# Kernel optimization log

Hardware: AMD Instinct MI355X
Metric: run time of the kernel (lower is better)

Reference implementation:

```python
import jax, jax.numpy as jnp
import numpy as np

L, B, S, H = 2, 32, 2048, 512  # layers, batch, src_len, hidden_size
D = 2 * H                      # feature dim of hidden / encoder_outputs


def setup_inputs() -> dict:
    key = jax.random.key(0)
    k1, k2, k3, k4, k5 = jax.random.split(key, 5)
    scale = 1.0 / np.sqrt(4 * H)
    return {
        "hidden": jax.random.normal(k1, (L, B, D), dtype=jnp.float32),
        "encoder_outputs": jax.random.normal(k2, (B, S, D), dtype=jnp.float32),
        "attn_w": jax.random.normal(k3, (H, 4 * H), dtype=jnp.float32) * scale,
        "attn_b": jax.random.normal(k4, (H,), dtype=jnp.float32) * scale,
        "v_w": jax.random.normal(k5, (1, H), dtype=jnp.float32) * (1.0 / np.sqrt(H)),
    }


def reference(hidden, encoder_outputs, attn_w, attn_b, v_w):
    # hidden: [L, B, D]; permute(1,0,2) then [:, -1, :] == last layer state [B, D]
    h = hidden[-1]  # [B, D]
    # Avoid materializing the [B,S,2D] concat: split attn_w into the block acting
    # on the (repeated) hidden part and the block acting on encoder_outputs.
    w_h, w_e = attn_w[:, :D], attn_w[:, D:]          # [H, D] each
    # hidden contribution is constant over src_len -> compute once per batch row
    e_h = jnp.einsum('bd,hd->bh', h, w_h)            # [B, H]
    e_e = jnp.einsum('bsd,hd->bsh', encoder_outputs, w_e)  # [B, S, H]
    energy = jnp.tanh(e_e + e_h[:, None, :] + attn_b)      # [B, S, H]
    scores = jnp.einsum('bsh,h->bs', energy, v_w[0])       # [B, S]
    attention_weights = jax.nn.softmax(scores, axis=1)     # [B, S]
    context = jnp.einsum('bs,bsd->bd', attention_weights, encoder_outputs)
    return (context[:, None, :], attention_weights[:, None, :])
```

## Files before the change

### kernel.cpp

```cpp
#include <hip/hip_runtime.h>
#include <math.h>

#define LL 2
#define BB 32
#define SS 2048
#define HH 512
#define DD 1024
#define W4S 2048

#define BM 64
#define BN 256
#define BK 64
#define NT (DD / BK)

typedef __attribute__((ext_vector_type(8))) short bf16x8;
typedef __attribute__((ext_vector_type(4))) float f32x4;

__device__ inline unsigned pk2_rne(float a, float b) {
    unsigned ua = __float_as_uint(a), ub = __float_as_uint(b);
    unsigned ra = (ua + 0x7fffu + ((ua >> 16) & 1u)) >> 16;
    unsigned rb = (ub + 0x7fffu + ((ub >> 16) & 1u)) & 0xffff0000u;
    return ra | rb;
}

__device__ inline unsigned pk2_hu(float a, float b) {
    unsigned ua = __float_as_uint(a) + 0x8000u;
    unsigned ub = __float_as_uint(b) + 0x8000u;
    return __builtin_amdgcn_perm(ub, ua, 0x07060302u);
}

__device__ inline float fast_tanh(float x) {
    x = fminf(9.f, fmaxf(-9.f, x));
    float e = __expf(2.f * x);
    return 1.f - 2.f * __builtin_amdgcn_rcpf(e + 1.f);
}

__device__ inline void gl_lds16(const unsigned short* g, short* l) {
    __builtin_amdgcn_global_load_lds(
        (const __attribute__((address_space(1))) unsigned int*)g,
        (__attribute__((address_space(3))) unsigned int*)l, 16, 0, 0);
}

__global__ __launch_bounds__(256) void k_prep(const float* __restrict__ hidden,
                                              const float* __restrict__ attn_w,
                                              const float* __restrict__ attn_b,
                                              unsigned short* __restrict__ Bp,
                                              float* __restrict__ base,
                                              float* __restrict__ scores) {
    int bx = blockIdx.x;
    if (bx < BB * SS / 256) {
        scores[bx * 256 + threadIdx.x] = 0.f;
        return;
    }
    bx -= BB * SS / 256;
    if (bx < HH) {
        int t = threadIdx.x;
        float4 v = *(const float4*)(attn_w + (size_t)bx * W4S + DD + t * 4);
        *(uint2*)(Bp + (size_t)bx * DD + t * 4) =
            make_uint2(pk2_rne(v.x, v.y), pk2_rne(v.z, v.w));
        return;
    }
    bx -= HH;
    int wid  = bx * 4 + (threadIdx.x >> 6);
    int lane = threadIdx.x & 63;
    int b = wid >> 9;
    int h = wid & (HH - 1);
    const float4* h4 = (const float4*)(hidden + (size_t)(LL - 1) * BB * DD + (size_t)b * DD);
    const float4* w4 = (const float4*)(attn_w + (size_t)h * W4S);
    float s = 0.f;
    #pragma unroll
    for (int i = 0; i < 4; i++) {
        float4 a = h4[lane + i * 64], w = w4[lane + i * 64];
        s += a.x * w.x + a.y * w.y + a.z * w.z + a.w * w.w;
    }
    #pragma unroll
    for (int off = 32; off; off >>= 1) s += __shfl_xor(s, off);
    if (lane == 0) base[b * HH + h] = s + attn_b[h];
}

__global__ __launch_bounds__(256, 2) void k_scores(const float* __restrict__ enc,
                                                   const unsigned short* __restrict__ Bp,
                                                   const float* __restrict__ base,
                                                   const float* __restrict__ vw,
                                                   float* __restrict__ scores) {
    __shared__ short As[2][8 * 64 * 8];
    __shared__ short Bs[2][4][8 * 64 * 8];

    const int tid  = threadIdx.x;
    const int wid  = tid >> 6;
    const int lane = tid & 63;
    const int lm   = lane & 15;
    const int kq   = lane >> 4;
    const int n0   = blockIdx.x * BN;
    const int m0   = blockIdx.y * BM;
    const int b    = m0 >> 11;
    const int wn   = n0 + wid * 64;

    const float* Ag = enc + (size_t)(m0 + wid * 16 + lm) * DD + kq * 8;
    const unsigned short* Bgl = Bp + (size_t)(wn + lm) * DD + kq * 8;

    #pragma unroll
    for (int ni = 0; ni < 4; ni++)
        #pragma unroll
        for (int s = 0; s < 2; s++)
            gl_lds16(Bgl + (size_t)ni * 16 * DD + s * 32,
                     &Bs[0][wid][(ni * 2 + s) * 64 * 8]);

    float4 ra[2][4];
    #pragma unroll
    for (int s = 0; s < 2; s++) {
        ra[0][s * 2 + 0] = *(const float4*)(Ag + s * 32);
        ra[0][s * 2 + 1] = *(const float4*)(Ag + s * 32 + 4);
        ra[1][s * 2 + 0] = *(const float4*)(Ag + 64 + s * 32);
        ra[1][s * 2 + 1] = *(const float4*)(Ag + 64 + s * 32 + 4);
    }
    #pragma unroll
    for (int s = 0; s < 2; s++) {
        float4 x = ra[0][s * 2], y = ra[0][s * 2 + 1];
        uint4 p = {pk2_hu(x.x, x.y), pk2_hu(x.z, x.w),
                   pk2_hu(y.x, y.y), pk2_hu(y.z, y.w)};
        *(uint4*)&As[0][((wid * 2 + s) * 64 + lane) * 8] = p;
    }

    f32x4 acc[4][4];
    #pragma unroll
    for (int i = 0; i < 4; i++)
        #pragma unroll
        for (int j = 0; j < 4; j++) acc[i][j] = (f32x4){0.f, 0.f, 0.f, 0.f};

    #pragma unroll 2
    for (int kt = 0; kt < NT; kt++) {
        const int c = kt & 1;
        __syncthreads();
        if (kt + 1 < NT) {
            #pragma unroll
            for (int ni = 0; ni < 4; ni++)
                #pragma unroll
                for (int s = 0; s < 2; s++)
                    gl_lds16(Bgl + (size_t)ni * 16 * DD + (kt + 1) * 64 + s * 32,
                             &Bs[c ^ 1][wid][(ni * 2 + s) * 64 * 8]);
            if (kt + 2 < NT) {
                #pragma unroll
                for (int s = 0; s < 2; s++) {
                    ra[c][s * 2 + 0] = *(const float4*)(Ag + (kt + 2) * 64 + s * 32);
                    ra[c][s * 2 + 1] = *(const float4*)(Ag + (kt + 2) * 64 + s * 32 + 4);
                }
            }
            #pragma unroll
            for (int s = 0; s < 2; s++) {
                float4 x = ra[c ^ 1][s * 2], y = ra[c ^ 1][s * 2 + 1];
                uint4 p = {pk2_hu(x.x, x.y), pk2_hu(x.z, x.w),
                           pk2_hu(y.x, y.y), pk2_hu(y.z, y.w)};
                *(uint4*)&As[c ^ 1][((wid * 2 + s) * 64 + lane) * 8] = p;
            }
        }
        #pragma unroll
        for (int s = 0; s < 2; s++) {
            bf16x8 af[4];
            #pragma unroll
            for (int mi = 0; mi < 4; mi++)
                af[mi] = *(const bf16x8*)&As[c][((mi * 2 + s) * 64 + lane) * 8];
            #pragma unroll
            for (int ni = 0; ni < 4; ni++) {
                bf16x8 bf = *(const bf16x8*)&Bs[c][wid][((ni * 2 + s) * 64 + lane) * 8];
                #pragma unroll
                for (int mi = 0; mi < 4; mi++)
                    acc[mi][ni] = __builtin_amdgcn_mfma_f32_16x16x32_bf16(
                        af[mi], bf, acc[mi][ni], 0, 0, 0);
            }
        }
    }

    const float* basep = base + b * HH + wn;
    const float* vp    = vw + wn;
    float p[4][4] = {};
    #pragma unroll
    for (int ni = 0; ni < 4; ni++) {
        int nl = ni * 16 + lm;
        float bs = basep[nl];
        float vv = vp[nl];
        #pragma unroll
        for (int mi = 0; mi < 4; mi++)
            #pragma unroll
            for (int r = 0; r < 4; r++)
                p[mi][r] += vv * fast_tanh(acc[mi][ni][r] + bs);
    }
    #pragma unroll
    for (int off = 8; off; off >>= 1)
        #pragma unroll
        for (int mi = 0; mi < 4; mi++)
            #pragma unroll
            for (int r = 0; r < 4; r++)
                p[mi][r] += __shfl_xor(p[mi][r], off);
    if (lm == 0) {
        #pragma unroll
        for (int mi = 0; mi < 4; mi++)
            #pragma unroll
            for (int r = 0; r < 4; r++)
                atomicAdd(&scores[m0 + mi * 16 + kq * 4 + r], p[mi][r]);
    }
}

__global__ __launch_bounds__(256) void k_smstat(const float* __restrict__ scores,
                                                float2* __restrict__ stat) {
    int b = blockIdx.x, tid = threadIdx.x;
    const float* rowp = scores + b * SS;
    float v[8];
    float m = -1e30f;
    #pragma unroll
    for (int i = 0; i < 8; i++) { v[i] = rowp[tid + i * 256]; m = fmaxf(m, v[i]); }
    __shared__ float sm[4], ssum[4];
    #pragma unroll
    for (int off = 32; off; off >>= 1) m = fmaxf(m, __shfl_xor(m, off));
    if ((tid & 63) == 0) sm[tid >> 6] = m;
    __syncthreads();
    m = fmaxf(fmaxf(sm[0], sm[1]), fmaxf(sm[2], sm[3]));
    float s = 0.f;
    #pragma unroll
    for (int i = 0; i < 8; i++) s += __expf(v[i] - m);
    #pragma unroll
    for (int off = 32; off; off >>= 1) s += __shfl_xor(s, off);
    if ((tid & 63) == 0) ssum[tid >> 6] = s;
    __syncthreads();
    if (tid == 0) {
        float tot = ssum[0] + ssum[1] + ssum[2] + ssum[3];
        stat[b] = make_float2(m, 1.f / tot);
    }
}

#define CCH 64
__global__ __launch_bounds__(256) void k_ctxpart(const float* __restrict__ enc,
                                                 const float* __restrict__ scores,
                                                 const float2* __restrict__ stat,
                                                 float* __restrict__ attn_out,
                                                 float* __restrict__ part) {
    int b = blockIdx.x, c = blockIdx.y, tid = threadIdx.x;
    __shared__ float wsh[CCH];
    float2 st = stat[b];
    if (tid < CCH) {
        float w = __expf(scores[b * SS + c * CCH + tid] - st.x) * st.y;
        wsh[tid] = w;
        attn_out[b * SS + c * CCH + tid] = w;
    }
    __syncthreads();
    const float4* e4 = (const float4*)(enc + ((size_t)b * SS + c * CCH) * DD);
    float4 acc = {0.f, 0.f, 0.f, 0.f};
    #pragma unroll 8
    for (int s = 0; s < CCH; s++) {
        float wv  = wsh[s];
        float4 ev = e4[(size_t)s * (DD / 4) + tid];
        acc.x += wv * ev.x; acc.y += wv * ev.y;
        acc.z += wv * ev.z; acc.w += wv * ev.w;
    }
    *(float4*)(part + (size_t)(b * 32 + c) * DD + tid * 4) = acc;
}

__global__ __launch_bounds__(256) void k_ctxreduce(const float* __restrict__ part,
                                                   float* __restrict__ ctx) {
    int b = blockIdx.x, d = blockIdx.y * 256 + threadIdx.x;
    float s = 0.f;
    #pragma unroll
    for (int c = 0; c < 32; c++) s += part[(size_t)(b * 32 + c) * DD + d];
    ctx[b * DD + d] = s;
}

extern "C" void kernel_launch(void* const* d_in, const int* in_sizes, int n_in,
                              void* d_out, int out_size, void* d_ws, size_t ws_size,
                              hipStream_t stream) {
    const float* hidden = (const float*)d_in[0];
    const float* enc    = (const float*)d_in[1];
    const float* attn_w = (const float*)d_in[2];
    const float* attn_b = (const float*)d_in[3];
    const float* v_w    = (const float*)d_in[4];

    float* out      = (float*)d_out;
    float* ctx_out  = out;
    float* attn_out = out + BB * DD;

    float* base        = (float*)d_ws;
    float* scores      = base + BB * HH;
    unsigned short* Bp = (unsigned short*)(scores + BB * SS);
    float2* stat       = (float2*)(Bp + (size_t)HH * DD);
    float* part        = (float*)(stat + BB);

    hipLaunchKernelGGL(k_prep, dim3(BB * SS / 256 + HH + BB * HH / 4), dim3(256),
                       0, stream, hidden, attn_w, attn_b, Bp, base, scores);
    hipLaunchKernelGGL(k_scores, dim3(2, BB * SS / BM), dim3(256), 0, stream,
                       enc, Bp, base, v_w, scores);
    hipLaunchKernelGGL(k_smstat, dim3(BB), dim3(256), 0, stream, scores, stat);
    hipLaunchKernelGGL(k_ctxpart, dim3(BB, SS / CCH), dim3(256), 0, stream,
                       enc, scores, stat, attn_out, part);
    hipLaunchKernelGGL(k_ctxreduce, dim3(BB, DD / 256), dim3(256), 0, stream,
                       part, ctx_out);
}
```

Before: 521.6 us.

## Retile scores GEMM with BK=32, pre-swizzled weight layout and higher occupancy

Repacks the bf16 weight matrix in the prep kernel into a k-tile-major layout with XOR swizzle, so each wave loads its B tile contiguously with global-to-LDS loads. The A tile load is restructured so each thread converts one float4 per row pair, writing into XOR-swizzled LDS to avoid bank conflicts. K-tile depth is halved to 32 and launch bounds raised to 4 blocks per CU, trading more loop iterations and barriers for smaller LDS use and higher occupancy to hide memory latency.

```diff
diff --git a/kernel.cpp b/kernel.cpp
--- a/kernel.cpp
+++ b/kernel.cpp
@@ -10,7 +10,7 @@
 
 #define BM 64
 #define BN 256
-#define BK 64
+#define BK 32
 #define NT (DD / BK)
 
 typedef __attribute__((ext_vector_type(8))) short bf16x8;
@@ -44,7 +44,7 @@
 __global__ __launch_bounds__(256) void k_prep(const float* __restrict__ hidden,
                                               const float* __restrict__ attn_w,
                                               const float* __restrict__ attn_b,
-                                              unsigned short* __restrict__ Bp,
+                                              unsigned short* __restrict__ BpT,
                                               float* __restrict__ base,
                                               float* __restrict__ scores) {
     int bx = blockIdx.x;
@@ -54,10 +54,12 @@
     }
     bx -= BB * SS / 256;
     if (bx < HH) {
-        int t = threadIdx.x;
-        float4 v = *(const float4*)(attn_w + (size_t)bx * W4S + DD + t * 4);
-        *(uint2*)(Bp + (size_t)bx * DD + t * 4) =
-            make_uint2(pk2_rne(v.x, v.y), pk2_rne(v.z, v.w));
+        int t = threadIdx.x, n = bx;
+        float4 v = *(const float4*)(attn_w + (size_t)n * W4S + DD + t * 4);
+        int kt = t >> 3, g = (t >> 1) & 3, half = t & 1;
+        size_t off = (size_t)kt * (512 * BK) + (size_t)n * BK
+                   + ((g ^ (n & 3)) * 8) + half * 4;
+        *(uint2*)(BpT + off) = make_uint2(pk2_rne(v.x, v.y), pk2_rne(v.z, v.w));
         return;
     }
     bx -= HH;
@@ -78,13 +80,13 @@
     if (lane == 0) base[b * HH + h] = s + attn_b[h];
 }
 
-__global__ __launch_bounds__(256, 2) void k_scores(const float* __restrict__ enc,
-                                                   const unsigned short* __restrict__ Bp,
+__global__ __launch_bounds__(256, 4) void k_scores(const float* __restrict__ enc,
+                                                   const unsigned short* __restrict__ BpT,
                                                    const float* __restrict__ base,
                                                    const float* __restrict__ vw,
                                                    float* __restrict__ scores) {
-    __shared__ short As[2][8 * 64 * 8];
-    __shared__ short Bs[2][4][8 * 64 * 8];
+    __shared__ short As[2][BM * BK];
+    __shared__ short Bs[2][BN * BK];
 
     const int tid  = threadIdx.x;
     const int wid  = tid >> 6;
@@ -96,31 +98,15 @@
     const int b    = m0 >> 11;
     const int wn   = n0 + wid * 64;
 
-    const float* Ag = enc + (size_t)(m0 + wid * 16 + lm) * DD + kq * 8;
-    const unsigned short* Bgl = Bp + (size_t)(wn + lm) * DD + kq * 8;
-
-    #pragma unroll
-    for (int ni = 0; ni < 4; ni++)
-        #pragma unroll
-        for (int s = 0; s < 2; s++)
-            gl_lds16(Bgl + (size_t)ni * 16 * DD + s * 32,
-                     &Bs[0][wid][(ni * 2 + s) * 64 * 8]);
-
-    float4 ra[2][4];
-    #pragma unroll
-    for (int s = 0; s < 2; s++) {
-        ra[0][s * 2 + 0] = *(const float4*)(Ag + s * 32);
-        ra[0][s * 2 + 1] = *(const float4*)(Ag + s * 32 + 4);
-        ra[1][s * 2 + 0] = *(const float4*)(Ag + 64 + s * 32);
-        ra[1][s * 2 + 1] = *(const float4*)(Ag + 64 + s * 32 + 4);
-    }
-    #pragma unroll
-    for (int s = 0; s < 2; s++) {
-        float4 x = ra[0][s * 2], y = ra[0][s * 2 + 1];
-        uint4 p = {pk2_hu(x.x, x.y), pk2_hu(x.z, x.w),
-                   pk2_hu(y.x, y.y), pk2_hu(y.z, y.w)};
-        *(uint4*)&As[0][((wid * 2 + s) * 64 + lane) * 8] = p;
-    }
+    const int rA = tid >> 3;
+    const int gA = tid & 7;
+    const float* Ag0 = enc + (size_t)(m0 + rA) * DD + gA * 4;
+    const float* Ag1 = Ag0 + (size_t)32 * DD;
+    const int wA0 = rA * BK + (((gA >> 1) ^ (rA & 3)) * 8) + (gA & 1) * 4;
+    const int wA1 = (rA + 32) * BK + (((gA >> 1) ^ ((rA + 32) & 3)) * 8) + (gA & 1) * 4;
+
+    const unsigned short* Bgw = BpT + (size_t)(n0 + wid * 64) * BK + lane * 8;
+    short* BsW[2] = { &Bs[0][wid * 64 * BK], &Bs[1][wid * 64 * BK] };
 
     f32x4 acc[4][4];
     #pragma unroll
@@ -128,46 +114,51 @@
         #pragma unroll
         for (int j = 0; j < 4; j++) acc[i][j] = (f32x4){0.f, 0.f, 0.f, 0.f};
 
-    #pragma unroll 2
+    #pragma unroll
+    for (int i = 0; i < 4; i++)
+        gl_lds16(Bgw + (size_t)i * 64 * 8, BsW[0] + i * 64 * 8);
+    float4 ra[2][2];
+    ra[0][0] = *(const float4*)(Ag0);
+    ra[0][1] = *(const float4*)(Ag1);
+    {
+        uint2 p0 = {pk2_hu(ra[0][0].x, ra[0][0].y), pk2_hu(ra[0][0].z, ra[0][0].w)};
+        uint2 p1 = {pk2_hu(ra[0][1].x, ra[0][1].y), pk2_hu(ra[0][1].z, ra[0][1].w)};
+        *(uint2*)&As[0][wA0] = p0;
+        *(uint2*)&As[0][wA1] = p1;
+    }
+    ra[1][0] = *(const float4*)(Ag0 + BK);
+    ra[1][1] = *(const float4*)(Ag1 + BK);
+
     for (int kt = 0; kt < NT; kt++) {
         const int c = kt & 1;
         __syncthreads();
         if (kt + 1 < NT) {
             #pragma unroll
-            for (int ni = 0; ni < 4; ni++)
-                #pragma unroll
-                for (int s = 0; s < 2; s++)
-                    gl_lds16(Bgl + (size_t)ni * 16 * DD + (kt + 1) * 64 + s * 32,
-                             &Bs[c ^ 1][wid][(ni * 2 + s) * 64 * 8]);
+            for (int i = 0; i < 4; i++)
+                gl_lds16(Bgw + (size_t)(kt + 1) * 512 * BK + (size_t)i * 64 * 8,
+                         BsW[c ^ 1] + i * 64 * 8);
+            float4 x = ra[c ^ 1][0], y = ra[c ^ 1][1];
+            uint2 p0 = {pk2_hu(x.x, x.y), pk2_hu(x.z, x.w)};
+            uint2 p1 = {pk2_hu(y.x, y.y), pk2_hu(y.z, y.w)};
+            *(uint2*)&As[c ^ 1][wA0] = p0;
+            *(uint2*)&As[c ^ 1][wA1] = p1;
             if (kt + 2 < NT) {
-                #pragma unroll
-                for (int s = 0; s < 2; s++) {
-                    ra[c][s * 2 + 0] = *(const float4*)(Ag + (kt + 2) * 64 + s * 32);
-                    ra[c][s * 2 + 1] = *(const float4*)(Ag + (kt + 2) * 64 + s * 32 + 4);
-                }
-            }
-            #pragma unroll
-            for (int s = 0; s < 2; s++) {
-                float4 x = ra[c ^ 1][s * 2], y = ra[c ^ 1][s * 2 + 1];
-                uint4 p = {pk2_hu(x.x, x.y), pk2_hu(x.z, x.w),
-                           pk2_hu(y.x, y.y), pk2_hu(y.z, y.w)};
-                *(uint4*)&As[c ^ 1][((wid * 2 + s) * 64 + lane) * 8] = p;
+                ra[c][0] = *(const float4*)(Ag0 + (kt + 2) * BK);
+                ra[c][1] = *(const float4*)(Ag1 + (kt + 2) * BK);
             }
         }
-        #pragma unroll
-        for (int s = 0; s < 2; s++) {
-            bf16x8 af[4];
+        bf16x8 af[4];
+        #pragma unroll
+        for (int mi = 0; mi < 4; mi++)
+            af[mi] = *(const bf16x8*)&As[c][(mi * 16 + lm) * BK + ((kq ^ (lm & 3)) * 8)];
+        #pragma unroll
+        for (int ni = 0; ni < 4; ni++) {
+            bf16x8 bf = *(const bf16x8*)
+                &Bs[c][(wid * 64 + ni * 16 + lm) * BK + ((kq ^ (lm & 3)) * 8)];
             #pragma unroll
             for (int mi = 0; mi < 4; mi++)
-                af[mi] = *(const bf16x8*)&As[c][((mi * 2 + s) * 64 + lane) * 8];
-            #pragma unroll
-            for (int ni = 0; ni < 4; ni++) {
-                bf16x8 bf = *(const bf16x8*)&Bs[c][wid][((ni * 2 + s) * 64 + lane) * 8];
-                #pragma unroll
-                for (int mi = 0; mi < 4; mi++)
-                    acc[mi][ni] = __builtin_amdgcn_mfma_f32_16x16x32_bf16(
-                        af[mi], bf, acc[mi][ni], 0, 0, 0);
-            }
+                acc[mi][ni] = __builtin_amdgcn_mfma_f32_16x16x32_bf16(
+                    af[mi], bf, acc[mi][ni], 0, 0, 0);
         }
     }
 
@@ -277,16 +268,16 @@
     float* ctx_out  = out;
     float* attn_out = out + BB * DD;
 
-    float* base        = (float*)d_ws;
-    float* scores      = base + BB * HH;
-    unsigned short* Bp = (unsigned short*)(scores + BB * SS);
-    float2* stat       = (float2*)(Bp + (size_t)HH * DD);
-    float* part        = (float*)(stat + BB);
+    float* base         = (float*)d_ws;
+    float* scores       = base + BB * HH;
+    unsigned short* BpT = (unsigned short*)(scores + BB * SS);
+    float2* stat        = (float2*)(BpT + (size_t)HH * DD);
+    float* part         = (float*)(stat + BB);
 
     hipLaunchKernelGGL(k_prep, dim3(BB * SS / 256 + HH + BB * HH / 4), dim3(256),
-                       0, stream, hidden, attn_w, attn_b, Bp, base, scores);
+                       0, stream, hidden, attn_w, attn_b, BpT, base, scores);
     hipLaunchKernelGGL(k_scores, dim3(2, BB * SS / BM), dim3(256), 0, stream,
-                       enc, Bp, base, v_w, scores);
+                       enc, BpT, base, v_w, scores);
     hipLaunchKernelGGL(k_smstat, dim3(BB), dim3(256), 0, stream, scores, stat);
     hipLaunchKernelGGL(k_ctxpart, dim3(BB, SS / CCH), dim3(256), 0, stream,
                        enc, scores, stat, attn_out, part);
```

New measurement: 599.0 us. +14.8%, slower.
